# Optimization experiments

Measured on AMD Instinct MI355X. Metric: run time of the kernel, lower is better.

The kernel has to match this reference:

```python
import jax, jax.numpy as jnp
import numpy as np

B, S, D = 2, 2048, 2048
NH, NKV = 32, 8
HD = D // NH           # 64
GS = NH // NKV         # 4
ROPE_BASE = 10000.0


def _rope_tables(seq_len, head_dim, base):
    inv_freq = 1.0 / (base ** (jnp.arange(head_dim // 2, dtype=jnp.float32) / (head_dim // 2)))
    angles = jnp.arange(seq_len, dtype=jnp.float32)[:, None] * inv_freq[None, :]  # [S, HD/2]
    angles = jnp.concatenate([angles, angles], axis=-1)                            # [S, HD]
    return jnp.cos(angles), jnp.sin(angles)


def _apply_rope(x, cos, sin):
    # x: [B, H, S, HD]
    hd = x.shape[-1]
    x1, x2 = x[..., : hd // 2], x[..., hd // 2 :]
    rotated = jnp.concatenate([-x2, x1], axis=-1)
    return (x * cos[None, None] + rotated * sin[None, None]).astype(x.dtype)


def setup_inputs() -> dict:
    key = jax.random.key(0)
    ks = jax.random.split(key, 5)
    scale = 0.02
    return {
        "x": jax.random.normal(ks[0], (B, S, D), dtype=jnp.float32),
        "Wq": jax.random.normal(ks[1], (D, D), dtype=jnp.float32) * scale,
        "Wk": jax.random.normal(ks[2], (D, NKV * HD), dtype=jnp.float32) * scale,
        "Wv": jax.random.normal(ks[3], (D, NKV * HD), dtype=jnp.float32) * scale,
        "Wo": jax.random.normal(ks[4], (D, D), dtype=jnp.float32) * scale,
    }


def reference(x, Wq, Wk, Wv, Wo):
    b, n, _ = x.shape
    cos, sin = _rope_tables(n, HD, ROPE_BASE)

    q = (x @ Wq).reshape(b, n, NH, HD).transpose(0, 2, 1, 3)    # [B, NH, S, HD]
    k = (x @ Wk).reshape(b, n, NKV, HD).transpose(0, 2, 1, 3)   # [B, NKV, S, HD]
    v = (x @ Wv).reshape(b, n, NKV, HD).transpose(0, 2, 1, 3)

    q = _apply_rope(q, cos, sin)
    k = _apply_rope(k, cos, sin)

    # GQA head sharing: repeat_interleave KV groups to full head count
    k = jnp.repeat(k, GS, axis=1)   # [B, NH, S, HD]
    v = jnp.repeat(v, GS, axis=1)

    scores = jnp.einsum("bhqd,bhkd->bhqk", q, k)                # [B, NH, S, S]
    causal = jnp.triu(jnp.ones((n, n), dtype=bool), k=1)
    scores = jnp.where(causal[None, None], -jnp.inf, scores)
    weights = jax.nn.softmax(scores / jnp.sqrt(jnp.float32(HD)), axis=-1)

    ctx = jnp.einsum("bhqk,bhkd->bhqd", weights, v)             # [B, NH, S, HD]
    ctx = ctx.transpose(0, 2, 1, 3).reshape(b, n, D)
    return ctx @ Wo
```

## Files before the change

### kernel.cpp

```cpp
#include <hip/hip_runtime.h>

typedef __bf16 bf16;
typedef __attribute__((ext_vector_type(8))) __bf16 bf16x8;
typedef __attribute__((ext_vector_type(4))) float f32x4;
typedef __attribute__((ext_vector_type(4))) short s16x4;

#define S_LEN 2048
#define D_MODEL 2048
#define NHEADS 32
#define NKVH 8
#define HDIM 64
#define BATCH 2

__device__ __forceinline__ void async_cp16(const bf16* g, bf16* l) {
    __builtin_amdgcn_global_load_lds(
        (const __attribute__((address_space(1))) unsigned int*)g,
        (__attribute__((address_space(3))) unsigned int*)l, 16, 0, 0);
}

__global__ void cvt_f32_bf16(const float* __restrict__ in, bf16* __restrict__ out, int n4) {
    int i = blockIdx.x * blockDim.x + threadIdx.x;
    if (i < n4) {
        float4 f = ((const float4*)in)[i];
        union { bf16 h[4]; uint2 u; } t;
        t.h[0] = (bf16)f.x; t.h[1] = (bf16)f.y; t.h[2] = (bf16)f.z; t.h[3] = (bf16)f.w;
        ((uint2*)out)[i] = t.u;
    }
}

__global__ void transpose_w(const float* __restrict__ W, bf16* __restrict__ Wt, int K, int N) {
    __shared__ float tile[32][33];
    int kt = blockIdx.y * 32, nt = blockIdx.x * 32;
    int tx = threadIdx.x, ty = threadIdx.y;
    #pragma unroll
    for (int i = 0; i < 32; i += 8)
        tile[ty + i][tx] = W[(size_t)(kt + ty + i) * N + nt + tx];
    __syncthreads();
    #pragma unroll
    for (int i = 0; i < 32; i += 8)
        Wt[(size_t)(nt + ty + i) * K + kt + tx] = (bf16)tile[tx][ty + i];
}

__global__ void transpose_v(const bf16* __restrict__ QKV, bf16* __restrict__ Vt) {
    __shared__ bf16 tl[32][33];
    int z = blockIdx.z;
    int s0 = blockIdx.x * 32, d0 = blockIdx.y * 32;
    int bb = z >> 3, hh = z & 7;
    int tx = threadIdx.x, ty = threadIdx.y;
    #pragma unroll
    for (int i = 0; i < 32; i += 8)
        tl[ty + i][tx] = QKV[((size_t)(bb * S_LEN + s0 + ty + i)) * 3072 + 2560 + hh * 64 + d0 + tx];
    __syncthreads();
    #pragma unroll
    for (int i = 0; i < 32; i += 8)
        Vt[((size_t)z * 64 + d0 + ty + i) * S_LEN + s0 + tx] = tl[tx][ty + i];
}

#define BUF1 16384

#define VMW(n) asm volatile("s_waitcnt vmcnt(" #n ")" ::: "memory")
#define BAR __builtin_amdgcn_s_barrier()

#define STAGE_A0(BUFOFF) do { \
    async_cp16(pa00, As + (BUFOFF) + la00); \
    async_cp16(pa01, As + (BUFOFF) + la01); \
    pa00 += 64; pa01 += 64; } while (0)
#define STAGE_A1(BUFOFF) do { \
    async_cp16(pa10, As + (BUFOFF) + la10); \
    async_cp16(pa11, As + (BUFOFF) + la11); \
    pa10 += 64; pa11 += 64; } while (0)
#define STAGE_B0(BUFOFF) do { \
    async_cp16(pb00, Bs + (BUFOFF) + lb00); \
    async_cp16(pb01, Bs + (BUFOFF) + lb01); \
    pb00 += 64; pb01 += 64; } while (0)
#define STAGE_B1(BUFOFF) do { \
    async_cp16(pb10, Bs + (BUFOFF) + lb10); \
    async_cp16(pb11, Bs + (BUFOFF) + lb11); \
    pb10 += 64; pb11 += 64; } while (0)

#define READ_A(QM, BUFOFF) do { \
    _Pragma("unroll") \
    for (int m_ = 0; m_ < 4; ++m_) { \
        const int row_ = wr * 128 + (QM) * 64 + m_ * 16 + l16; \
        af[m_][0] = *(const bf16x8*)&As[(BUFOFF) + row_ * 64 + ((quad ^ sw8) * 8)]; \
        af[m_][1] = *(const bf16x8*)&As[(BUFOFF) + row_ * 64 + (((4 + quad) ^ sw8) * 8)]; \
    } } while (0)

#define READ_B(QN, BUFOFF, BV) do { \
    _Pragma("unroll") \
    for (int n_ = 0; n_ < 2; ++n_) { \
        const int row_ = wc * 64 + (QN) * 32 + n_ * 16 + l16; \
        BV[n_][0] = *(const bf16x8*)&Bs[(BUFOFF) + row_ * 64 + ((quad ^ sw8) * 8)]; \
        BV[n_][1] = *(const bf16x8*)&Bs[(BUFOFF) + row_ * 64 + (((4 + quad) ^ sw8) * 8)]; \
    } } while (0)

#define MFMA_Q(QM, QN, BV) do { \
    _Pragma("unroll") \
    for (int kk_ = 0; kk_ < 2; ++kk_) \
        _Pragma("unroll") \
        for (int m_ = 0; m_ < 4; ++m_) \
            _Pragma("unroll") \
            for (int n_ = 0; n_ < 2; ++n_) \
                acc[(QM) * 4 + m_][(QN) * 2 + n_] = __builtin_amdgcn_mfma_f32_16x16x32_bf16( \
                    af[m_][kk_], BV[n_][kk_], acc[(QM) * 4 + m_][(QN) * 2 + n_], 0, 0, 0); \
    } while (0)

#define SYNCM(QM, QN, BV) do { \
    BAR; \
    __builtin_amdgcn_s_setprio(1); \
    MFMA_Q(QM, QN, BV); \
    __builtin_amdgcn_s_setprio(0); } while (0)

#define TILE_S(CUR) do { \
    READ_A(0, CUR); READ_B(0, CUR, bfr0);             SYNCM(0, 0, bfr0); BAR; \
    STAGE_A0(CUR); STAGE_B0(CUR); READ_B(1, CUR, bfr1); SYNCM(0, 1, bfr1); BAR; \
    STAGE_B1(CUR); READ_A(1, CUR);                    SYNCM(1, 0, bfr0); BAR; \
    STAGE_A1(CUR);                                    SYNCM(1, 1, bfr1); VMW(8); BAR; } while (0)

#define TILE_N(CUR, W) do { \
    READ_A(0, CUR); READ_B(0, CUR, bfr0); SYNCM(0, 0, bfr0); BAR; \
    READ_B(1, CUR, bfr1);                 SYNCM(0, 1, bfr1); BAR; \
    READ_A(1, CUR);                       SYNCM(1, 0, bfr0); BAR; \
                                          SYNCM(1, 1, bfr1); W; BAR; } while (0)

template <bool OUT_BF16>
__global__ __launch_bounds__(512, 2) void gemm256(const bf16* __restrict__ A,
                                                  const bf16* __restrict__ Bt,
                                                  void* __restrict__ Cv,
                                                  int N, int K) {
    __shared__ __align__(16) bf16 As[2 * 256 * 64];
    __shared__ __align__(16) bf16 Bs[2 * 256 * 64];

    const int tid  = threadIdx.x;
    const int w    = tid >> 6;
    const int lane = tid & 63;
    const int l16  = lane & 15;
    const int quad = lane >> 4;
    const int sw8  = l16 & 7;
    const int wr   = w >> 2;
    const int wc   = w & 3;

    const int nbx  = N >> 8;
    const int nwg  = gridDim.x;
    const int orig = blockIdx.x;
    const int wg   = (orig & 7) * (nwg >> 3) + (orig >> 3);
    const int n0   = (wg % nbx) * 256;
    const int m0   = (wg / nbx) * 256;

    const int krow = lane >> 3;
    const int kc   = (lane & 7) ^ krow;

    const bf16* pa00 = A + (size_t)(m0 +   0 + w * 8 + krow) * K + kc * 8;
    const bf16* pa01 = A + (size_t)(m0 + 128 + w * 8 + krow) * K + kc * 8;
    const bf16* pa10 = A + (size_t)(m0 +  64 + w * 8 + krow) * K + kc * 8;
    const bf16* pa11 = A + (size_t)(m0 + 192 + w * 8 + krow) * K + kc * 8;
    const int brow0 = (w >> 2) * 64 + (w & 3) * 8 + krow;
    const bf16* pb00 = Bt + (size_t)(n0 +       brow0) * K + kc * 8;
    const bf16* pb01 = Bt + (size_t)(n0 + 128 + brow0) * K + kc * 8;
    const bf16* pb10 = Bt + (size_t)(n0 +  32 + brow0) * K + kc * 8;
    const bf16* pb11 = Bt + (size_t)(n0 + 160 + brow0) * K + kc * 8;

    const int la00 = w * 512;
    const int la01 = 8192 + w * 512;
    const int la10 = 4096 + w * 512;
    const int la11 = 12288 + w * 512;
    const int lbb  = ((w >> 2) * 64 + (w & 3) * 8) * 64;
    const int lb00 = lbb;
    const int lb01 = 8192 + lbb;
    const int lb10 = 2048 + lbb;
    const int lb11 = 10240 + lbb;

    f32x4 acc[8][4];
    #pragma unroll
    for (int i = 0; i < 8; ++i)
        #pragma unroll
        for (int j = 0; j < 4; ++j) acc[i][j] = (f32x4){0.f, 0.f, 0.f, 0.f};

    bf16x8 af[4][2];
    bf16x8 bfr0[2][2];
    bf16x8 bfr1[2][2];

    STAGE_A0(0); STAGE_B0(0); STAGE_B1(0); STAGE_A1(0);
    STAGE_A0(BUF1); STAGE_B0(BUF1); STAGE_B1(BUF1); STAGE_A1(BUF1);
    VMW(8);
    BAR;

    const int NITER = K >> 6;
    for (int it = 0; it < (NITER - 2) >> 1; ++it) {
        TILE_S(0);
        TILE_S(BUF1);
    }
    TILE_N(0, VMW(0));
    TILE_N(BUF1, );

    #pragma unroll
    for (int mi = 0; mi < 8; ++mi)
        #pragma unroll
        for (int ni = 0; ni < 4; ++ni)
            #pragma unroll
            for (int r = 0; r < 4; ++r) {
                size_t row = (size_t)(m0 + wr * 128 + mi * 16 + quad * 4 + r);
                size_t col = (size_t)(n0 + wc * 64 + ni * 16 + l16);
                if (OUT_BF16) ((bf16*)Cv)[row * N + col] = (bf16)acc[mi][ni][r];
                else          ((float*)Cv)[row * N + col] = acc[mi][ni][r];
            }
}

__global__ void rope_relayout(const bf16* __restrict__ QKV,
                              bf16* __restrict__ Qr, bf16* __restrict__ Kr) {
    const int QN = BATCH * S_LEN * NHEADS * 32;
    const int KN = BATCH * S_LEN * NKVH * 32;
    const float LC = 0.28782313662425572f;
    int idx = blockIdx.x * 256 + threadIdx.x;
    if (idx < QN) {
        int j = idx & 31, hh = (idx >> 5) & 31, s = (idx >> 10) & 2047, bb = idx >> 21;
        size_t src = ((size_t)(bb * S_LEN + s)) * 3072 + hh * HDIM + j;
        float x1 = (float)QKV[src], x2 = (float)QKV[src + 32];
        float ang = (float)s * __expf(-(float)j * LC);
        float sn, cs; sincosf(ang, &sn, &cs);
        size_t dst = ((size_t)((bb * NHEADS + hh) * S_LEN + s)) * HDIM + j;
        Qr[dst]      = (bf16)((x1 * cs - x2 * sn) * 0.125f);
        Qr[dst + 32] = (bf16)((x2 * cs + x1 * sn) * 0.125f);
    } else if (idx < QN + KN) {
        int t = idx - QN;
        int j = t & 31, hh = (t >> 5) & 7, s = (t >> 8) & 2047, bb = t >> 19;
        size_t src = ((size_t)(bb * S_LEN + s)) * 3072 + 2048 + hh * HDIM + j;
        float x1 = (float)QKV[src], x2 = (float)QKV[src + 32];
        float ang = (float)s * __expf(-(float)j * LC);
        float sn, cs; sincosf(ang, &sn, &cs);
        size_t dst = ((size_t)((bb * NKVH + hh) * S_LEN + s)) * HDIM + j;
        Kr[dst]      = (bf16)(x1 * cs - x2 * sn);
        Kr[dst + 32] = (bf16)(x2 * cs + x1 * sn);
    }
}

__global__ __launch_bounds__(256, 3) void attn_kernel(const bf16* __restrict__ Q,
                                                      const bf16* __restrict__ K,
                                                      const bf16* __restrict__ Vt,
                                                      bf16* __restrict__ Ctx) {
    __shared__ __align__(16) bf16 KsL[128 * 64];
    __shared__ __align__(16) bf16 VtL[64 * 128];

    static const signed char QTAB[16] = {15,14,13,12, 10,11,8,9, 5,4,7,6, 0,1,2,3};
    const int bx = blockIdx.x;
    const int qt = QTAB[((bx >> 8) << 2) | ((bx >> 6) & 3)];
    const int bh = bx & 63;
    const int b  = bh >> 5;
    const int h  = bh & 31;
    const int kvh = h >> 2;
    const int tid = threadIdx.x;
    const int wave = tid >> 6;
    const int lane = tid & 63;
    const int l16  = lane & 15;
    const int quad = lane >> 4;

    const bf16* Qb = Q  + ((size_t)(b * NHEADS + h)) * S_LEN * HDIM;
    const bf16* Kb = K  + ((size_t)(b * NKVH + kvh)) * S_LEN * HDIM;
    const bf16* Vb = Vt + ((size_t)(b * NKVH + kvh)) * HDIM * S_LEN;

    const int q0 = qt * 128;

    bf16x8 aq[2][2];
    #pragma unroll
    for (int qf = 0; qf < 2; ++qf)
        #pragma unroll
        for (int ks = 0; ks < 2; ++ks)
            aq[qf][ks] = *(const bf16x8*)(Qb + (size_t)(q0 + wave * 32 + qf * 16 + l16) * HDIM + ks * 32 + quad * 8);

    f32x4 O[2][4];
    float M0 = -1e30f, M1 = -1e30f;
    float l0 = 0.f, l1 = 0.f;
    #pragma unroll
    for (int qf = 0; qf < 2; ++qf)
        #pragma unroll
        for (int df = 0; df < 4; ++df) O[qf][df] = (f32x4){0.f,0.f,0.f,0.f};

    const int krow = lane >> 3, kslot = lane & 7;
    const int kc   = kslot ^ (krow & 7);
    const int vslot = lane & 15, vsub = lane >> 4;

    #pragma unroll 1
    for (int kt = 0; kt <= qt; ++kt) {
        const int k0 = kt * 128;
        __syncthreads();
        #pragma unroll
        for (int j = 0; j < 4; ++j) {
            int rbase = (wave * 4 + j) * 8;
            async_cp16(Kb + (size_t)(k0 + rbase + krow) * HDIM + kc * 8, &KsL[rbase * 64]);
            int d0 = (wave * 4 + j) * 4;
            int vrow = d0 + vsub;
            int vc = vslot ^ (vrow & 15);
            async_cp16(Vb + (size_t)vrow * S_LEN + k0 + vc * 8, &VtL[d0 * 128]);
        }
        __syncthreads();

        f32x4 sc[2][8];
        #pragma unroll
        for (int kf = 0; kf < 8; ++kf) {
            sc[0][kf] = (f32x4){0.f,0.f,0.f,0.f};
            sc[1][kf] = (f32x4){0.f,0.f,0.f,0.f};
            #pragma unroll
            for (int ks = 0; ks < 2; ++ks) {
                bf16x8 bk = *(const bf16x8*)&KsL[(kf * 16 + l16) * 64 + (((ks * 4 + quad) ^ (l16 & 7)) * 8)];
                sc[0][kf] = __builtin_amdgcn_mfma_f32_16x16x32_bf16(bk, aq[0][ks], sc[0][kf], 0, 0, 0);
                sc[1][kf] = __builtin_amdgcn_mfma_f32_16x16x32_bf16(bk, aq[1][ks], sc[1][kf], 0, 0, 0);
            }
        }

        if (kt == qt) {
            #pragma unroll
            for (int kf = 0; kf < 8; ++kf)
                #pragma unroll
                for (int r = 0; r < 4; ++r) {
                    int key = kf * 16 + quad * 4 + r;
                    int qi0 = wave * 32 + l16;
                    if (key > qi0)      sc[0][kf][r] = -1e30f;
                    if (key > qi0 + 16) sc[1][kf][r] = -1e30f;
                }
        }

        float mx0 = sc[0][0][0], mx1 = sc[1][0][0];
        #pragma unroll
        for (int kf = 0; kf < 8; ++kf)
            #pragma unroll
            for (int r = 0; r < 4; ++r) {
                mx0 = fmaxf(mx0, sc[0][kf][r]);
                mx1 = fmaxf(mx1, sc[1][kf][r]);
            }
        mx0 = fmaxf(mx0, __shfl_xor(mx0, 16)); mx0 = fmaxf(mx0, __shfl_xor(mx0, 32));
        mx1 = fmaxf(mx1, __shfl_xor(mx1, 16)); mx1 = fmaxf(mx1, __shfl_xor(mx1, 32));

        float Mn0 = fmaxf(M0, mx0), Mn1 = fmaxf(M1, mx1);
        float a0 = __expf(M0 - Mn0), a1 = __expf(M1 - Mn1);
        M0 = Mn0; M1 = Mn1;
        l0 *= a0; l1 *= a1;

        #pragma unroll
        for (int r = 0; r < 4; ++r) {
            float aO0 = __shfl(a0, quad * 4 + r);
            float aO1 = __shfl(a1, quad * 4 + r);
            #pragma unroll
            for (int df = 0; df < 4; ++df) {
                O[0][df][r] *= aO0;
                O[1][df][r] *= aO1;
            }
        }

        #pragma unroll
        for (int kf = 0; kf < 8; ++kf)
            #pragma unroll
            for (int r = 0; r < 4; ++r) {
                float e0 = __expf(sc[0][kf][r] - M0); sc[0][kf][r] = e0; l0 += e0;
                float e1 = __expf(sc[1][kf][r] - M1); sc[1][kf][r] = e1; l1 += e1;
            }

        #pragma unroll
        for (int kf = 0; kf < 8; ++kf) {
            union { bf16 hh[4]; s16x4 s4; } p0, p1;
            #pragma unroll
            for (int r = 0; r < 4; ++r) {
                p0.hh[r] = (bf16)sc[0][kf][r];
                p1.hh[r] = (bf16)sc[1][kf][r];
            }
            #pragma unroll
            for (int df = 0; df < 4; ++df) {
                s16x4 bv = *(const s16x4*)&VtL[(df * 16 + l16) * 128 +
                                               (((kf * 2 + (quad >> 1)) ^ l16) * 8) + (quad & 1) * 4];
                O[0][df] = __builtin_amdgcn_mfma_f32_16x16x16bf16_1k(p0.s4, bv, O[0][df], 0, 0, 0);
                O[1][df] = __builtin_amdgcn_mfma_f32_16x16x16bf16_1k(p1.s4, bv, O[1][df], 0, 0, 0);
            }
        }
    }

    l0 += __shfl_xor(l0, 16); l0 += __shfl_xor(l0, 32);
    l1 += __shfl_xor(l1, 16); l1 += __shfl_xor(l1, 32);
    #pragma unroll
    for (int r = 0; r < 4; ++r) {
        float inv0 = 1.0f / __shfl(l0, quad * 4 + r);
        float inv1 = 1.0f / __shfl(l1, quad * 4 + r);
        size_t row0 = (size_t)b * S_LEN + q0 + wave * 32 + quad * 4 + r;
        bf16* dst0 = Ctx + row0 * D_MODEL + h * HDIM;
        bf16* dst1 = dst0 + (size_t)16 * D_MODEL;
        #pragma unroll
        for (int df = 0; df < 4; ++df) {
            dst0[df * 16 + l16] = (bf16)(O[0][df][r] * inv0);
            dst1[df * 16 + l16] = (bf16)(O[1][df][r] * inv1);
        }
    }
}

extern "C" void kernel_launch(void* const* d_in, const int* in_sizes, int n_in,
                              void* d_out, int out_size, void* d_ws, size_t ws_size,
                              hipStream_t stream) {
    const float* x  = (const float*)d_in[0];
    const float* Wq = (const float*)d_in[1];
    const float* Wk = (const float*)d_in[2];
    const float* Wv = (const float*)d_in[3];
    const float* Wo = (const float*)d_in[4];

    char* p = (char*)d_ws;
    bf16* X16 = (bf16*)p; p += (size_t)4096 * 2048 * 2;
    bf16* WqT = (bf16*)p; p += (size_t)2048 * 2048 * 2;
    bf16* WkT = (bf16*)p; p += (size_t)512 * 2048 * 2;
    bf16* WvT = (bf16*)p; p += (size_t)512 * 2048 * 2;
    bf16* WoT = (bf16*)p; p += (size_t)2048 * 2048 * 2;
    bf16* QKV = (bf16*)p; p += (size_t)4096 * 3072 * 2;
    bf16* Qr  = (bf16*)p; p += (size_t)4096 * 2048 * 2;
    bf16* Kr  = (bf16*)p; p += (size_t)4096 * 512 * 2;
    bf16* Vt  = (bf16*)p; p += (size_t)16 * 64 * 2048 * 2;
    bf16* Ctx = QKV;

    cvt_f32_bf16<<<8192, 256, 0, stream>>>(x, X16, 2097152);
    transpose_w<<<dim3(64, 64), dim3(32, 8), 0, stream>>>(Wq, WqT, 2048, 2048);
    transpose_w<<<dim3(16, 64), dim3(32, 8), 0, stream>>>(Wk, WkT, 2048, 512);
    transpose_w<<<dim3(16, 64), dim3(32, 8), 0, stream>>>(Wv, WvT, 2048, 512);
    transpose_w<<<dim3(64, 64), dim3(32, 8), 0, stream>>>(Wo, WoT, 2048, 2048);

    gemm256<true><<<dim3(192), 512, 0, stream>>>(X16, WqT, (void*)QKV, 4096 == 0 ? 0 : 3072, 2048);

    rope_relayout<<<20480, 256, 0, stream>>>(QKV, Qr, Kr);
    transpose_v<<<dim3(64, 2, 16), dim3(32, 8), 0, stream>>>(QKV, Vt);
    attn_kernel<<<1024, 256, 0, stream>>>(Qr, Kr, Vt, Ctx);

    gemm256<false><<<dim3(128), 512, 0, stream>>>(Ctx, WoT, d_out, 2048, 2048);
}
```

Measured before the change: 321.9 us.

## Merge preprocessing launches, fuse RoPE with V transpose, use 128x128 GEMM for output

Merges the x conversion and four weight transposes into one preproc launch, and merges the RoPE relayout with the V transpose into one rope_tv launch, cutting the number of kernel launches and the tail gaps between them. It also replaces the 256-tile output projection GEMM (128 blocks) with a simpler single-buffered 128x128-tile gemm_bt (512 blocks), so that more of the GPU's compute units get work. The new GEMM has no double buffering and syncs twice per k-step, so its per-block efficiency may be lower.

```diff
diff --git a/kernel.cpp b/kernel.cpp
--- a/kernel.cpp
+++ b/kernel.cpp
@@ -18,20 +18,31 @@
         (__attribute__((address_space(3))) unsigned int*)l, 16, 0, 0);
 }
 
-__global__ void cvt_f32_bf16(const float* __restrict__ in, bf16* __restrict__ out, int n4) {
-    int i = blockIdx.x * blockDim.x + threadIdx.x;
-    if (i < n4) {
-        float4 f = ((const float4*)in)[i];
+__global__ void preproc(const float* __restrict__ x,
+                        const float* __restrict__ Wq, const float* __restrict__ Wk,
+                        const float* __restrict__ Wv, const float* __restrict__ Wo,
+                        bf16* __restrict__ X16, bf16* __restrict__ WqT, bf16* __restrict__ WkT,
+                        bf16* __restrict__ WvT, bf16* __restrict__ WoT) {
+    __shared__ float tile[32][33];
+    const int tid = threadIdx.x;
+    int bid = blockIdx.x;
+    if (bid < 8192) {
+        int i = bid * 256 + tid;
+        float4 f = ((const float4*)x)[i];
         union { bf16 h[4]; uint2 u; } t;
         t.h[0] = (bf16)f.x; t.h[1] = (bf16)f.y; t.h[2] = (bf16)f.z; t.h[3] = (bf16)f.w;
-        ((uint2*)out)[i] = t.u;
-    }
-}
-
-__global__ void transpose_w(const float* __restrict__ W, bf16* __restrict__ Wt, int K, int N) {
-    __shared__ float tile[32][33];
-    int kt = blockIdx.y * 32, nt = blockIdx.x * 32;
-    int tx = threadIdx.x, ty = threadIdx.y;
+        ((uint2*)X16)[i] = t.u;
+        return;
+    }
+    int l = bid - 8192;
+    const float* W; bf16* Wt; int N, bx, by;
+    const int K = 2048;
+    if (l < 4096)      {            W = Wq; Wt = WqT; N = 2048; bx = l & 63; by = l >> 6; }
+    else if (l < 5120) { l -= 4096; W = Wk; Wt = WkT; N = 512;  bx = l & 15; by = l >> 4; }
+    else if (l < 6144) { l -= 5120; W = Wv; Wt = WvT; N = 512;  bx = l & 15; by = l >> 4; }
+    else               { l -= 6144; W = Wo; Wt = WoT; N = 2048; bx = l & 63; by = l >> 6; }
+    const int kt = by * 32, nt = bx * 32;
+    const int tx = tid & 31, ty = tid >> 5;
     #pragma unroll
     for (int i = 0; i < 32; i += 8)
         tile[ty + i][tx] = W[(size_t)(kt + ty + i) * N + nt + tx];
@@ -41,19 +52,84 @@
         Wt[(size_t)(nt + ty + i) * K + kt + tx] = (bf16)tile[tx][ty + i];
 }
 
-__global__ void transpose_v(const bf16* __restrict__ QKV, bf16* __restrict__ Vt) {
-    __shared__ bf16 tl[32][33];
-    int z = blockIdx.z;
-    int s0 = blockIdx.x * 32, d0 = blockIdx.y * 32;
-    int bb = z >> 3, hh = z & 7;
-    int tx = threadIdx.x, ty = threadIdx.y;
-    #pragma unroll
-    for (int i = 0; i < 32; i += 8)
-        tl[ty + i][tx] = QKV[((size_t)(bb * S_LEN + s0 + ty + i)) * 3072 + 2560 + hh * 64 + d0 + tx];
-    __syncthreads();
-    #pragma unroll
-    for (int i = 0; i < 32; i += 8)
-        Vt[((size_t)z * 64 + d0 + ty + i) * S_LEN + s0 + tx] = tl[tx][ty + i];
+template <bool OUT_BF16>
+__global__ __launch_bounds__(256) void gemm_bt(const bf16* __restrict__ A,
+                                               const bf16* __restrict__ Bt,
+                                               void* __restrict__ Cv,
+                                               int M, int N, int K) {
+    __shared__ __align__(16) bf16 As[128 * 64];
+    __shared__ __align__(16) bf16 Bs[128 * 64];
+
+    const int tid  = threadIdx.x;
+    const int wave = tid >> 6;
+    const int lane = tid & 63;
+    const int l16  = lane & 15;
+    const int quad = lane >> 4;
+    const int wrow = (wave >> 1) * 64;
+    const int wcol = (wave & 1) * 64;
+    const int m0 = blockIdx.y * 128;
+    const int n0 = blockIdx.x * 128;
+
+    const int krow = lane >> 3;
+    const int kc   = (lane & 7) ^ krow;
+    const bf16* gA = A  + (size_t)(m0 + wave * 32 + krow) * K + kc * 8;
+    const bf16* gB = Bt + (size_t)(n0 + wave * 32 + krow) * K + kc * 8;
+    bf16* lA = &As[wave * 2048];
+    bf16* lB = &Bs[wave * 2048];
+    const size_t rstep = (size_t)8 * K;
+
+    const int sw = l16 & 7;
+
+    f32x4 acc[4][4];
+    #pragma unroll
+    for (int mi = 0; mi < 4; ++mi)
+        #pragma unroll
+        for (int ni = 0; ni < 4; ++ni)
+            acc[mi][ni] = (f32x4){0.f, 0.f, 0.f, 0.f};
+
+    for (int k0 = 0; k0 < K; k0 += 64) {
+        __syncthreads();
+        async_cp16(gA,             lA);
+        async_cp16(gA +     rstep, lA + 512);
+        async_cp16(gA + 2 * rstep, lA + 1024);
+        async_cp16(gA + 3 * rstep, lA + 1536);
+        async_cp16(gB,             lB);
+        async_cp16(gB +     rstep, lB + 512);
+        async_cp16(gB + 2 * rstep, lB + 1024);
+        async_cp16(gB + 3 * rstep, lB + 1536);
+        gA += 64; gB += 64;
+        __syncthreads();
+
+        #pragma unroll
+        for (int kk = 0; kk < 2; ++kk) {
+            bf16x8 af[4], bfr[4];
+            #pragma unroll
+            for (int mi = 0; mi < 4; ++mi)
+                af[mi] = *(const bf16x8*)&As[(wrow + mi * 16 + l16) * 64 + (((kk * 4 + quad) ^ sw) * 8)];
+            #pragma unroll
+            for (int ni = 0; ni < 4; ++ni)
+                bfr[ni] = *(const bf16x8*)&Bs[(wcol + ni * 16 + l16) * 64 + (((kk * 4 + quad) ^ sw) * 8)];
+            #pragma unroll
+            for (int mi = 0; mi < 4; ++mi)
+                #pragma unroll
+                for (int ni = 0; ni < 4; ++ni)
+                    acc[mi][ni] = __builtin_amdgcn_mfma_f32_16x16x32_bf16(af[mi], bfr[ni], acc[mi][ni], 0, 0, 0);
+        }
+    }
+
+    #pragma unroll
+    for (int mi = 0; mi < 4; ++mi) {
+        #pragma unroll
+        for (int ni = 0; ni < 4; ++ni) {
+            #pragma unroll
+            for (int r = 0; r < 4; ++r) {
+                size_t row = (size_t)(m0 + wrow + mi * 16 + quad * 4 + r);
+                size_t col = (size_t)(n0 + wcol + ni * 16 + l16);
+                if (OUT_BF16) ((bf16*)Cv)[row * N + col] = (bf16)acc[mi][ni][r];
+                else          ((float*)Cv)[row * N + col] = acc[mi][ni][r];
+            }
+        }
+    }
 }
 
 #define BUF1 16384
@@ -206,32 +282,51 @@
             }
 }
 
-__global__ void rope_relayout(const bf16* __restrict__ QKV,
-                              bf16* __restrict__ Qr, bf16* __restrict__ Kr) {
-    const int QN = BATCH * S_LEN * NHEADS * 32;
-    const int KN = BATCH * S_LEN * NKVH * 32;
+__global__ void rope_tv(const bf16* __restrict__ QKV,
+                        bf16* __restrict__ Qr, bf16* __restrict__ Kr,
+                        bf16* __restrict__ Vt) {
+    __shared__ bf16 tl[32][33];
+    const int tid = threadIdx.x;
+    const int bid = blockIdx.x;
     const float LC = 0.28782313662425572f;
-    int idx = blockIdx.x * 256 + threadIdx.x;
-    if (idx < QN) {
-        int j = idx & 31, hh = (idx >> 5) & 31, s = (idx >> 10) & 2047, bb = idx >> 21;
-        size_t src = ((size_t)(bb * S_LEN + s)) * 3072 + hh * HDIM + j;
-        float x1 = (float)QKV[src], x2 = (float)QKV[src + 32];
-        float ang = (float)s * __expf(-(float)j * LC);
-        float sn, cs; sincosf(ang, &sn, &cs);
-        size_t dst = ((size_t)((bb * NHEADS + hh) * S_LEN + s)) * HDIM + j;
-        Qr[dst]      = (bf16)((x1 * cs - x2 * sn) * 0.125f);
-        Qr[dst + 32] = (bf16)((x2 * cs + x1 * sn) * 0.125f);
-    } else if (idx < QN + KN) {
-        int t = idx - QN;
-        int j = t & 31, hh = (t >> 5) & 7, s = (t >> 8) & 2047, bb = t >> 19;
-        size_t src = ((size_t)(bb * S_LEN + s)) * 3072 + 2048 + hh * HDIM + j;
-        float x1 = (float)QKV[src], x2 = (float)QKV[src + 32];
-        float ang = (float)s * __expf(-(float)j * LC);
-        float sn, cs; sincosf(ang, &sn, &cs);
-        size_t dst = ((size_t)((bb * NKVH + hh) * S_LEN + s)) * HDIM + j;
-        Kr[dst]      = (bf16)(x1 * cs - x2 * sn);
-        Kr[dst + 32] = (bf16)(x2 * cs + x1 * sn);
-    }
+    if (bid < 20480) {
+        const int QN = BATCH * S_LEN * NHEADS * 32;
+        int idx = bid * 256 + tid;
+        if (idx < QN) {
+            int j = idx & 31, hh = (idx >> 5) & 31, s = (idx >> 10) & 2047, bb = idx >> 21;
+            size_t src = ((size_t)(bb * S_LEN + s)) * 3072 + hh * HDIM + j;
+            float x1 = (float)QKV[src], x2 = (float)QKV[src + 32];
+            float ang = (float)s * __expf(-(float)j * LC);
+            float sn, cs; sincosf(ang, &sn, &cs);
+            size_t dst = ((size_t)((bb * NHEADS + hh) * S_LEN + s)) * HDIM + j;
+            Qr[dst]      = (bf16)((x1 * cs - x2 * sn) * 0.125f);
+            Qr[dst + 32] = (bf16)((x2 * cs + x1 * sn) * 0.125f);
+        } else {
+            int t = idx - QN;
+            int j = t & 31, hh = (t >> 5) & 7, s = (t >> 8) & 2047, bb = t >> 19;
+            size_t src = ((size_t)(bb * S_LEN + s)) * 3072 + 2048 + hh * HDIM + j;
+            float x1 = (float)QKV[src], x2 = (float)QKV[src + 32];
+            float ang = (float)s * __expf(-(float)j * LC);
+            float sn, cs; sincosf(ang, &sn, &cs);
+            size_t dst = ((size_t)((bb * NKVH + hh) * S_LEN + s)) * HDIM + j;
+            Kr[dst]      = (bf16)(x1 * cs - x2 * sn);
+            Kr[dst + 32] = (bf16)(x2 * cs + x1 * sn);
+        }
+        return;
+    }
+    int l = bid - 20480;
+    int s0 = (l & 63) * 32;
+    int d0 = ((l >> 6) & 1) * 32;
+    int z  = l >> 7;
+    int bb = z >> 3, hh = z & 7;
+    int tx = tid & 31, ty = tid >> 5;
+    #pragma unroll
+    for (int i = 0; i < 32; i += 8)
+        tl[ty + i][tx] = QKV[((size_t)(bb * S_LEN + s0 + ty + i)) * 3072 + 2560 + hh * 64 + d0 + tx];
+    __syncthreads();
+    #pragma unroll
+    for (int i = 0; i < 32; i += 8)
+        Vt[((size_t)z * 64 + d0 + ty + i) * S_LEN + s0 + tx] = tl[tx][ty + i];
 }
 
 __global__ __launch_bounds__(256, 3) void attn_kernel(const bf16* __restrict__ Q,
@@ -410,17 +505,13 @@
     bf16* Vt  = (bf16*)p; p += (size_t)16 * 64 * 2048 * 2;
     bf16* Ctx = QKV;
 
-    cvt_f32_bf16<<<8192, 256, 0, stream>>>(x, X16, 2097152);
-    transpose_w<<<dim3(64, 64), dim3(32, 8), 0, stream>>>(Wq, WqT, 2048, 2048);
-    transpose_w<<<dim3(16, 64), dim3(32, 8), 0, stream>>>(Wk, WkT, 2048, 512);
-    transpose_w<<<dim3(16, 64), dim3(32, 8), 0, stream>>>(Wv, WvT, 2048, 512);
-    transpose_w<<<dim3(64, 64), dim3(32, 8), 0, stream>>>(Wo, WoT, 2048, 2048);
-
-    gemm256<true><<<dim3(192), 512, 0, stream>>>(X16, WqT, (void*)QKV, 4096 == 0 ? 0 : 3072, 2048);
-
-    rope_relayout<<<20480, 256, 0, stream>>>(QKV, Qr, Kr);
-    transpose_v<<<dim3(64, 2, 16), dim3(32, 8), 0, stream>>>(QKV, Vt);
+    preproc<<<18432, 256, 0, stream>>>(x, Wq, Wk, Wv, Wo, X16, WqT, WkT, WvT, WoT);
+
+    gemm256<true><<<dim3(192), 512, 0, stream>>>(X16, WqT, (void*)QKV, 3072, 2048);
+
+    rope_tv<<<22528, 256, 0, stream>>>(QKV, Qr, Kr, Vt);
+
     attn_kernel<<<1024, 256, 0, stream>>>(Qr, Kr, Vt, Ctx);
 
-    gemm256<false><<<dim3(128), 512, 0, stream>>>(Ctx, WoT, d_out, 2048, 2048);
-}
+    gemm_bt<false><<<dim3(16, 32), 256, 0, stream>>>(Ctx, WoT, d_out, 4096, 2048, 2048);
+}
```

Result: faster. 291.8 us (-9.3%).
